# Kernel tuning notes

Measured on AMD Instinct MI355X. Metric: run time of the kernel, lower is better.

The kernel has to match this reference:

```python
import jax, jax.numpy as jnp
import numpy as np

D_MODEL = 1024


def setup_inputs() -> dict:
    key = jax.random.key(0)
    ks = jax.random.split(key, 7)
    B, S, D = 4, 2048, D_MODEL
    scale = 1.0 / np.sqrt(D)
    inp = {
        "query": jax.random.normal(ks[0], (B, S, D), dtype=jnp.float32),
        "key": jax.random.normal(ks[1], (B, S, D), dtype=jnp.float32),
        "value": jax.random.normal(ks[2], (B, S, D), dtype=jnp.float32),
        # NOTE: original torch code applies query_projection to q, k AND v,
        # so only one projection weight (Wq) participates, plus output proj.
        "Wq": (jax.random.normal(ks[3], (D, D), dtype=jnp.float32) * scale),
        "bq": jnp.zeros((D,), dtype=jnp.float32),
        "Wo": (jax.random.normal(ks[4], (D, D), dtype=jnp.float32) * scale),
        "bo": jnp.zeros((D,), dtype=jnp.float32),
    }
    return inp


def reference(query, key, value, Wq, bq, Wo, bo):
    # Faithful to source: same projection (Wq, bq) used for q, k, v.
    q = jnp.einsum("bsd,de->bse", query, Wq) + bq   # (B, S, D)
    k = jnp.einsum("btd,de->bte", key, Wq) + bq     # (B, T, D)
    v = jnp.einsum("btd,de->bte", value, Wq) + bq   # (B, T, D)
    # No 1/sqrt(d) scaling in the original.
    score = jnp.einsum("bse,bte->bst", q, k)        # (B, S, T)
    weights = jax.nn.softmax(score, axis=-1)
    # Dropout is identity in eval / for a deterministic reference.
    ctx = jnp.einsum("bst,bte->bse", weights, v)    # (B, S, D)
    out = jnp.einsum("bse,ef->bsf", ctx, Wo) + bo   # (B, S, D)
    return (out, weights)
```

## Files before the change

kernel.cpp:

```cpp
#include <hip/hip_runtime.h>

typedef unsigned short u16;
typedef unsigned int u32;
typedef signed char i8;
typedef __bf16 bf16x8 __attribute__((ext_vector_type(8)));
typedef float f32x4 __attribute__((ext_vector_type(4)));
typedef int i32x4 __attribute__((ext_vector_type(4)));
typedef i8 i8x4 __attribute__((ext_vector_type(4)));

#define AS1(p) ((const __attribute__((address_space(1))) void*)(p))
#define AS3(p) ((__attribute__((address_space(3))) void*)(p))

__device__ __forceinline__ u16 f2bf(float x) {
  u32 u = __float_as_uint(x);
  u32 r = u + 0x7fffu + ((u >> 16) & 1u);
  return (u16)(r >> 16);
}
__device__ __forceinline__ float bf2f(u16 h) {
  return __uint_as_float(((u32)h) << 16);
}

#define S_IN (8.0f / 127.0f)
#define S_W (0.25f / 127.0f)
#define S_QK (8.0f / 127.0f)
#define INV_S_IN (127.0f / 8.0f)
#define INV_S_W (508.0f)
#define INV_S_QK (127.0f / 8.0f)

__device__ __forceinline__ int2 q8i(float x, float inv_s) {
  float t = fminf(fmaxf(x * inv_s, -126.99f), 126.99f);
  float hf = rintf(t);
  float lf = fminf(fmaxf(rintf((t - hf) * 256.0f), -127.0f), 127.0f);
  return make_int2((int)hf, (int)lf);
}

__global__ __launch_bounds__(256) void split_qk_i8(
    const float* __restrict__ q, const float* __restrict__ k,
    i8* __restrict__ qh, i8* __restrict__ ql, i8* __restrict__ kh,
    i8* __restrict__ kl, int n4) {
  int stride = gridDim.x * blockDim.x;
  for (int i = blockIdx.x * blockDim.x + threadIdx.x; i < n4; i += stride) {
    float4 x = ((const float4*)q)[i];
    float xs[4] = {x.x, x.y, x.z, x.w};
    i8x4 h, l;
#pragma unroll
    for (int e = 0; e < 4; ++e) {
      int2 r = q8i(xs[e], INV_S_IN);
      h[e] = (i8)r.x;
      l[e] = (i8)r.y;
    }
    ((i8x4*)qh)[i] = h;
    ((i8x4*)ql)[i] = l;
    x = ((const float4*)k)[i];
    float ys[4] = {x.x, x.y, x.z, x.w};
#pragma unroll
    for (int e = 0; e < 4; ++e) {
      int2 r = q8i(ys[e], INV_S_IN);
      h[e] = (i8)r.x;
      l[e] = (i8)r.y;
    }
    ((i8x4*)kh)[i] = h;
    ((i8x4*)kl)[i] = l;
  }
}

__global__ void prep_w_i8(const float* __restrict__ Wq,
                          const float* __restrict__ Wo, i8* __restrict__ wqt_h,
                          i8* __restrict__ wqt_l, u16* __restrict__ wot,
                          u16* __restrict__ wq_b, int D) {
  __shared__ float tq[32][33];
  __shared__ float to[32][33];
  int c0 = blockIdx.x * 32, r0 = blockIdx.y * 32;
  int tx = threadIdx.x, ty = threadIdx.y;
#pragma unroll
  for (int i = ty; i < 32; i += 8) {
    float xq = Wq[(size_t)(r0 + i) * D + c0 + tx];
    tq[i][tx] = xq;
    wq_b[(size_t)(r0 + i) * D + c0 + tx] = f2bf(xq);
    to[i][tx] = Wo[(size_t)(r0 + i) * D + c0 + tx];
  }
  __syncthreads();
#pragma unroll
  for (int i = ty; i < 32; i += 8) {
    float x = tq[tx][i];
    int2 r = q8i(x, INV_S_W);
    size_t o = (size_t)(c0 + i) * D + r0 + tx;
    wqt_h[o] = (i8)r.x;
    wqt_l[o] = (i8)r.y;
    wot[o] = f2bf(to[tx][i]);
  }
}

__global__ void transpose_f32_bf16(const float* __restrict__ in,
                                   u16* __restrict__ out, int R, int C) {
  __shared__ float tile[32][33];
  size_t zi = (size_t)blockIdx.z * R * C;
  int c0 = blockIdx.x * 32, r0 = blockIdx.y * 32;
  int tx = threadIdx.x, ty = threadIdx.y;
#pragma unroll
  for (int i = ty; i < 32; i += 8)
    tile[i][tx] = in[zi + (size_t)(r0 + i) * C + (c0 + tx)];
  __syncthreads();
#pragma unroll
  for (int i = ty; i < 32; i += 8)
    out[zi + (size_t)(c0 + i) * R + (r0 + tx)] = f2bf(tile[tx][i]);
}

__global__ __launch_bounds__(256) void bqo_kernel(const float* __restrict__ bq,
                                                  const u16* __restrict__ wot,
                                                  const float* __restrict__ bo,
                                                  float* __restrict__ bqo,
                                                  int D) {
  const int f = blockIdx.x * 4 + (threadIdx.x >> 6);
  const int lane = threadIdx.x & 63;
  const u16* wr_ = wot + (size_t)f * D;
  float s = 0.f;
  for (int e = lane; e < D; e += 64) s += bq[e] * bf2f(wr_[e]);
#pragma unroll
  for (int off = 32; off; off >>= 1) s += __shfl_xor(s, off);
  if (lane == 0) bqo[f] = s + bo[f];
}

template <int EPI>
__global__ __launch_bounds__(256, 2) void gemm_bt(
    const u16* __restrict__ Ah, const u16* __restrict__ Bh,
    const float* __restrict__ bias, float* __restrict__ Cf,
    u16* __restrict__ Ch, int M, int N, int K,
    long long sA, long long sB, long long sC) {
  __shared__ alignas(16) u16 As[128 * 32];
  __shared__ alignas(16) u16 Bs[128 * 32];

  const int t = threadIdx.x;
  const int lane = t & 63;
  const int w = t >> 6;
  const int wr = w >> 1, wc = w & 1;

  const long long zb = blockIdx.z;
  const u16* pA = Ah + zb * sA;
  const u16* pB = Bh + zb * sB;

  const int m0 = blockIdx.x * 128;
  const int n0 = blockIdx.y * 128;

  f32x4 acc[4][4] = {};

  const int row0 = t >> 2;
  const int colS = (t & 3) * 8;
  const int lds0 = (t & ~63) * 8;
  const int lds1 = (256 + (t & ~63)) * 8;

  const size_t aoff0 = (size_t)(m0 + row0) * K + colS;
  const size_t aoff1 = (size_t)(m0 + row0 + 64) * K + colS;
  const size_t boff0 = (size_t)(n0 + row0) * K + colS;
  const size_t boff1 = (size_t)(n0 + row0 + 64) * K + colS;

  for (int k0 = 0; k0 < K; k0 += 32) {
    __syncthreads();
    __builtin_amdgcn_global_load_lds(AS1(pA + aoff0 + k0), AS3(&As[lds0]), 16, 0, 0);
    __builtin_amdgcn_global_load_lds(AS1(pA + aoff1 + k0), AS3(&As[lds1]), 16, 0, 0);
    __builtin_amdgcn_global_load_lds(AS1(pB + boff0 + k0), AS3(&Bs[lds0]), 16, 0, 0);
    __builtin_amdgcn_global_load_lds(AS1(pB + boff1 + k0), AS3(&Bs[lds1]), 16, 0, 0);
    __syncthreads();

    const int fr = lane & 15;
    const int kc = (lane >> 4) * 8;
    bf16x8 a[4], b[4];
#pragma unroll
    for (int i = 0; i < 4; ++i)
      a[i] = *(const bf16x8*)&As[(wr * 64 + i * 16 + fr) * 32 + kc];
#pragma unroll
    for (int j = 0; j < 4; ++j)
      b[j] = *(const bf16x8*)&Bs[(wc * 64 + j * 16 + fr) * 32 + kc];
#pragma unroll
    for (int i = 0; i < 4; ++i)
#pragma unroll
      for (int j = 0; j < 4; ++j)
        acc[i][j] = __builtin_amdgcn_mfma_f32_16x16x32_bf16(a[i], b[j], acc[i][j], 0, 0, 0);
  }

  const int er = (lane >> 4) * 4;
  const int ec = lane & 15;
#pragma unroll
  for (int j = 0; j < 4; ++j) {
    const int gcol = n0 + wc * 64 + j * 16 + ec;
    const float bv = bias ? bias[gcol] : 0.0f;
#pragma unroll
    for (int i = 0; i < 4; ++i) {
      const int grow0 = m0 + wr * 64 + i * 16 + er;
#pragma unroll
      for (int r = 0; r < 4; ++r) {
        const float x = acc[i][j][r] + bv;
        const size_t off = (size_t)zb * sC + (size_t)(grow0 + r) * N + gcol;
        if constexpr (EPI == 0) Cf[off] = x;
        else Ch[off] = f2bf(x);
      }
    }
  }
}

#define PH_PRE()                                                               \
  __builtin_amdgcn_s_barrier();                                                \
  asm volatile("s_waitcnt lgkmcnt(0)" ::: "memory");                           \
  __builtin_amdgcn_s_setprio(1)

#define PH_POST()                                                              \
  __builtin_amdgcn_s_setprio(0);                                               \
  __builtin_amdgcn_s_barrier()

#define STG_I(DSTBASE, SH, SL, ROWBASE, KREAL)                                 \
  do {                                                                         \
    const i8* s0_ = (sc < 4 ? (SH) : (SL)) +                                   \
                    (size_t)((ROWBASE) + sr) * K + (KREAL) + ((sc & 3) << 4);  \
    const i8* s1_ = s0_ + (size_t)64 * K;                                      \
    __builtin_amdgcn_global_load_lds(AS1(s0_), AS3(&lds8[(DSTBASE) + ldsB]), 16, 0, 0); \
    __builtin_amdgcn_global_load_lds(AS1(s1_), AS3(&lds8[(DSTBASE) + 8192 + ldsB]), 16, 0, 0); \
  } while (0)

#define LDA_I(BUF, QM)                                                         \
  do {                                                                         \
    const int base_ = (BUF) * 49152;                                           \
    _Pragma("unroll") for (int i_ = 0; i_ < 4; ++i_) {                         \
      const int r_ = (QM) * 128 + wr * 64 + i_ * 16 + fr;                      \
      ah_[i_] = *(const i32x4*)&lds8[base_ + r_ * 128 + ((ksl ^ (r_ & 7)) << 4)]; \
      al_[i_] = *(const i32x4*)&lds8[base_ + r_ * 128 + (((4 + ksl) ^ (r_ & 7)) << 4)]; \
    }                                                                          \
  } while (0)

#define LDB_I(BUF, J, BH, BL)                                                  \
  do {                                                                         \
    const int base_ = (BUF) * 49152 + 32768;                                   \
    const int r_ = wc * 32 + (J) * 16 + fr;                                    \
    BH = *(const i32x4*)&lds8[base_ + r_ * 128 + ((ksl ^ (r_ & 7)) << 4)];     \
    BL = *(const i32x4*)&lds8[base_ + r_ * 128 + (((4 + ksl) ^ (r_ & 7)) << 4)]; \
  } while (0)

#define MMA_I(QM, J, BH, BL)                                                   \
  do {                                                                         \
    _Pragma("unroll") for (int i_ = 0; i_ < 4; ++i_) {                         \
      accH[(QM) * 4 + i_][J] = __builtin_amdgcn_mfma_i32_16x16x64_i8(          \
          ah_[i_], BH, accH[(QM) * 4 + i_][J], 0, 0, 0);                       \
      accX[(QM) * 4 + i_][J] = __builtin_amdgcn_mfma_i32_16x16x64_i8(          \
          ah_[i_], BL, accX[(QM) * 4 + i_][J], 0, 0, 0);                       \
      accX[(QM) * 4 + i_][J] = __builtin_amdgcn_mfma_i32_16x16x64_i8(          \
          al_[i_], BH, accX[(QM) * 4 + i_][J], 0, 0, 0);                       \
    }                                                                          \
  } while (0)

template <int EPI>
__global__ __launch_bounds__(512, 2) void gemm8i(
    const i8* __restrict__ Ah, const i8* __restrict__ Al,
    const i8* __restrict__ Bh, const i8* __restrict__ Bl,
    const float* __restrict__ bias, float sAB, float* __restrict__ Cf,
    i8* __restrict__ Ch, i8* __restrict__ Cl, int M, int N, int K,
    long long sA, long long sB, long long sC) {
  extern __shared__ i8 lds8[];

  const int tt = threadIdx.x;
  const int lane = tt & 63;
  const int wv = tt >> 6;
  const int wr = wv >> 2;
  const int wc = wv & 3;
  const int fr = lane & 15;
  const int ksl = lane >> 4;

  const long long zb = blockIdx.z;
  const i8* pAh = Ah + zb * sA;
  const i8* pAl = Al + zb * sA;
  const i8* pBh = Bh + zb * sB;
  const i8* pBl = Bl + zb * sB;
  const int m0 = blockIdx.x * 256;
  const int n0 = blockIdx.y * 128;

  const int sr = tt >> 3;
  const int ss = tt & 7;
  const int sc = ss ^ (sr & 7);
  const int ldsB = (tt & ~63) * 16;

  i32x4 accH[8][2] = {};
  i32x4 accX[8][2] = {};
  i32x4 ah_[4], al_[4], b0h, b0l, b1h, b1l;

  const int NT = K / 64;
  const int NITER = NT / 2;

  STG_I(0, pAh, pAl, m0, 0);
  STG_I(16384, pAh, pAl, m0 + 128, 0);
  STG_I(32768, pBh, pBl, n0, 0);
  STG_I(49152, pAh, pAl, m0, 64);
  asm volatile("s_waitcnt vmcnt(2)" ::: "memory");
  __builtin_amdgcn_s_barrier();
  __builtin_amdgcn_sched_barrier(0);

  for (int it = 0; it < NITER; ++it) {
    const int t0 = 2 * it;
    const int k1 = (t0 + 1) * 64;
    const int k2 = (t0 + 2 < NT ? t0 + 2 : NT - 1) * 64;
    const int k3 = (t0 + 3 < NT ? t0 + 3 : NT - 1) * 64;

    LDA_I(0, 0);
    LDB_I(0, 0, b0h, b0l);
    STG_I(49152 + 16384, pAh, pAl, m0 + 128, k1);
    PH_PRE();
    MMA_I(0, 0, b0h, b0l);
    PH_POST();

    LDB_I(0, 1, b1h, b1l);
    STG_I(49152 + 32768, pBh, pBl, n0, k1);
    PH_PRE();
    MMA_I(0, 1, b1h, b1l);
    PH_POST();

    LDA_I(0, 1);
    STG_I(0, pAh, pAl, m0, k2);
    PH_PRE();
    MMA_I(1, 0, b0h, b0l);
    PH_POST();

    PH_PRE();
    MMA_I(1, 1, b1h, b1l);
    __builtin_amdgcn_s_setprio(0);
    asm volatile("s_waitcnt vmcnt(2)" ::: "memory");
    __builtin_amdgcn_s_barrier();
    __builtin_amdgcn_sched_barrier(0);

    LDA_I(1, 0);
    LDB_I(1, 0, b0h, b0l);
    STG_I(16384, pAh, pAl, m0 + 128, k2);
    PH_PRE();
    MMA_I(0, 0, b0h, b0l);
    PH_POST();

    LDB_I(1, 1, b1h, b1l);
    STG_I(32768, pBh, pBl, n0, k2);
    PH_PRE();
    MMA_I(0, 1, b1h, b1l);
    PH_POST();

    LDA_I(1, 1);
    STG_I(49152, pAh, pAl, m0, k3);
    PH_PRE();
    MMA_I(1, 0, b0h, b0l);
    PH_POST();

    PH_PRE();
    MMA_I(1, 1, b1h, b1l);
    __builtin_amdgcn_s_setprio(0);
    asm volatile("s_waitcnt vmcnt(2)" ::: "memory");
    __builtin_amdgcn_s_barrier();
    __builtin_amdgcn_sched_barrier(0);
  }

  const int er = (lane >> 4) * 4;
  const int ec = lane & 15;
#pragma unroll
  for (int fi = 0; fi < 8; ++fi) {
    const int grow0 = m0 + (fi >> 2) * 128 + wr * 64 + (fi & 3) * 16 + er;
#pragma unroll
    for (int j = 0; j < 2; ++j) {
      const int gcol = n0 + wc * 32 + j * 16 + ec;
      const float bv = bias ? bias[gcol] : 0.0f;
#pragma unroll
      for (int r = 0; r < 4; ++r) {
        const float x =
            sAB * ((float)accH[fi][j][r] + (float)accX[fi][j][r] * 0.00390625f) + bv;
        const size_t off = (size_t)zb * sC + (size_t)(grow0 + r) * N + gcol;
        if constexpr (EPI == 0) {
          Cf[off] = x;
        } else {
          int2 qq = q8i(x, INV_S_QK);
          Ch[off] = (i8)qq.x;
          Cl[off] = (i8)qq.y;
        }
      }
    }
  }
}

#define STG_P(DSTBASE, SRC, ROWBASE, KREAL)                                    \
  do {                                                                         \
    const u16* s0_ = (SRC) + (size_t)((ROWBASE) + sr) * K + (KREAL) + (sc << 3); \
    const u16* s1_ = s0_ + (size_t)64 * K;                                     \
    __builtin_amdgcn_global_load_lds(AS1(s0_), AS3(&lds[(DSTBASE) + ldsW]), 16, 0, 0); \
    __builtin_amdgcn_global_load_lds(AS1(s1_), AS3(&lds[(DSTBASE) + 4096 + ldsW]), 16, 0, 0); \
  } while (0)

#define LDA_P(BUF, QM, S)                                                      \
  do {                                                                         \
    const int base_ = (BUF) * 24576 + (QM) * 8192;                             \
    _Pragma("unroll") for (int i_ = 0; i_ < 4; ++i_) {                         \
      const int r_ = wr * 64 + i_ * 16 + fr;                                   \
      a[i_] = *(const bf16x8*)&lds[base_ + r_ * 64 + (((((S) * 4 + ksl)) ^ (r_ & 7)) << 3)]; \
    }                                                                          \
  } while (0)

#define LDB_P(BUF, S)                                                          \
  do {                                                                         \
    const int base_ = (BUF) * 24576 + 16384;                                   \
    _Pragma("unroll") for (int j_ = 0; j_ < 2; ++j_) {                         \
      const int r_ = wc * 32 + j_ * 16 + fr;                                   \
      b[j_] = *(const bf16x8*)&lds[base_ + r_ * 64 + (((((S) * 4 + ksl)) ^ (r_ & 7)) << 3)]; \
    }                                                                          \
  } while (0)

#define MMA_P(QM)                                                              \
  do {                                                                         \
    _Pragma("unroll") for (int i_ = 0; i_ < 4; ++i_) {                         \
      _Pragma("unroll") for (int j_ = 0; j_ < 2; ++j_) {                       \
        acc[(QM) * 4 + i_][j_] = __builtin_amdgcn_mfma_f32_16x16x32_bf16(      \
            a[i_], b[j_], acc[(QM) * 4 + i_][j_], 0, 0, 0);                    \
      }                                                                        \
    }                                                                          \
  } while (0)

template <int EPI>
__global__ __launch_bounds__(512, 2) void gemm8p(
    const u16* __restrict__ A, const u16* __restrict__ B,
    const float* __restrict__ bias, float* __restrict__ Cf,
    u16* __restrict__ Ch, int M, int N, int K,
    long long sA, long long sB, long long sC) {
  extern __shared__ u16 lds[];

  const int tt = threadIdx.x;
  const int lane = tt & 63;
  const int wv = tt >> 6;
  const int wr = wv >> 2;
  const int wc = wv & 3;
  const int fr = lane & 15;
  const int ksl = lane >> 4;

  const long long zb = blockIdx.z;
  const u16* pA = A + zb * sA;
  const u16* pB = B + zb * sB;
  const int m0 = blockIdx.x * 256;
  const int n0 = blockIdx.y * 128;

  const int sr = tt >> 3;
  const int ss = tt & 7;
  const int sc = ss ^ (sr & 7);
  const int ldsW = (tt & ~63) * 8;

  f32x4 acc[8][2] = {};
  bf16x8 a[4], b[2];

  const int NT = K / 64;

  STG_P(16384, pB, n0, 0);
  STG_P(0, pA, m0, 0);
  STG_P(8192, pA, m0 + 128, 0);
  asm volatile("s_waitcnt vmcnt(2)" ::: "memory");
  __builtin_amdgcn_s_barrier();
  __builtin_amdgcn_sched_barrier(0);

  for (int it = 0; it < NT; ++it) {
    const int cur = it & 1;
    const int nb = (cur ^ 1) * 24576;
    const int kn = (it + 1 < NT ? it + 1 : NT - 1) * 64;

    LDA_P(cur, 0, 0);
    LDB_P(cur, 0);
    STG_P(nb + 16384, pB, n0, kn);
    PH_PRE();
    MMA_P(0);
    __builtin_amdgcn_s_setprio(0);
    asm volatile("s_waitcnt vmcnt(2)" ::: "memory");
    __builtin_amdgcn_s_barrier();
    __builtin_amdgcn_sched_barrier(0);

    LDA_P(cur, 1, 0);
    STG_P(nb + 0, pA, m0, kn);
    PH_PRE();
    MMA_P(1);
    PH_POST();

    LDA_P(cur, 0, 1);
    LDB_P(cur, 1);
    STG_P(nb + 8192, pA, m0 + 128, kn);
    PH_PRE();
    MMA_P(0);
    PH_POST();

    LDA_P(cur, 1, 1);
    PH_PRE();
    MMA_P(1);
    __builtin_amdgcn_s_setprio(0);
    asm volatile("s_waitcnt vmcnt(2)" ::: "memory");
    __builtin_amdgcn_s_barrier();
    __builtin_amdgcn_sched_barrier(0);
  }

  const int er = (lane >> 4) * 4;
  const int ec = lane & 15;
#pragma unroll
  for (int fi = 0; fi < 8; ++fi) {
    const int qm = fi >> 2, i = fi & 3;
    const int grow0 = m0 + qm * 128 + wr * 64 + i * 16 + er;
#pragma unroll
    for (int j = 0; j < 2; ++j) {
      const int gcol = n0 + wc * 32 + j * 16 + ec;
      const float bv = bias ? bias[gcol] : 0.0f;
#pragma unroll
      for (int r = 0; r < 4; ++r) {
        const float x = acc[fi][j][r] + bv;
        const size_t off = (size_t)zb * sC + (size_t)(grow0 + r) * N + gcol;
        if constexpr (EPI == 0) Cf[off] = x;
        else Ch[off] = f2bf(x);
      }
    }
  }
}

__global__ __launch_bounds__(256) void softmax_rows(float* __restrict__ S,
                                                    u16* __restrict__ P) {
  const int T = 2048;
  const size_t row = blockIdx.x;
  float* sr = S + row * T;
  u16* pr = P + row * T;
  const int t = threadIdx.x;
  const int w = t >> 6, lane = t & 63;
  __shared__ float red[8];

  float v[8];
  float mx = -1e30f;
#pragma unroll
  for (int i = 0; i < 8; ++i) {
    v[i] = sr[t + 256 * i];
    mx = fmaxf(mx, v[i]);
  }
#pragma unroll
  for (int off = 32; off; off >>= 1) mx = fmaxf(mx, __shfl_xor(mx, off));
  if (lane == 0) red[w] = mx;
  __syncthreads();
  mx = fmaxf(fmaxf(red[0], red[1]), fmaxf(red[2], red[3]));

  float s = 0.f;
#pragma unroll
  for (int i = 0; i < 8; ++i) {
    v[i] = __expf(v[i] - mx);
    s += v[i];
  }
#pragma unroll
  for (int off = 32; off; off >>= 1) s += __shfl_xor(s, off);
  if (lane == 0) red[4 + w] = s;
  __syncthreads();
  s = (red[4] + red[5]) + (red[6] + red[7]);
  const float inv = 1.0f / s;
#pragma unroll
  for (int i = 0; i < 8; ++i) {
    const float wv = v[i] * inv;
    sr[t + 256 * i] = wv;
    pr[t + 256 * i] = f2bf(wv);
  }
}

extern "C" void kernel_launch(void* const* d_in, const int* in_sizes, int n_in,
                              void* d_out, int out_size, void* d_ws,
                              size_t ws_size, hipStream_t stream) {
  (void)in_sizes; (void)n_in; (void)out_size; (void)ws_size;
  const float* query = (const float*)d_in[0];
  const float* key   = (const float*)d_in[1];
  const float* value = (const float*)d_in[2];
  const float* Wq    = (const float*)d_in[3];
  const float* bq    = (const float*)d_in[4];
  const float* Wo    = (const float*)d_in[5];
  const float* bo    = (const float*)d_in[6];

  const int S = 2048, D = 1024;
  const size_t n = (size_t)4 * S * D;

  float* out = (float*)d_out;
  float* wts = out + n;

  char* ws = (char*)d_ws;
  i8* wqt_h = (i8*)(ws);
  i8* wqt_l = (i8*)(ws + (1ull << 20));
  u16* wot  = (u16*)(ws + (2ull << 20));
  u16* wq_b = (u16*)(ws + (4ull << 20));
  u16* wqoT = (u16*)(ws + (6ull << 20));
  float* bqo = (float*)(ws + (8ull << 20));
  i8* QKh = (i8*)(ws + (9ull << 20));
  i8* QKl = (i8*)(ws + (25ull << 20));
  u16* tmp = (u16*)(ws + (41ull << 20));
  u16* P = (u16*)(ws + (9ull << 20));

  i8* ah = (i8*)wts;
  i8* al = ah + 2 * n;
  u16* valT = (u16*)out;

  hipFuncSetAttribute((const void*)&gemm8i<2>,
                      hipFuncAttributeMaxDynamicSharedMemorySize, 98304);
  hipFuncSetAttribute((const void*)&gemm8i<0>,
                      hipFuncAttributeMaxDynamicSharedMemorySize, 98304);
  hipFuncSetAttribute((const void*)&gemm8p<1>,
                      hipFuncAttributeMaxDynamicSharedMemorySize, 98304);
  hipFuncSetAttribute((const void*)&gemm8p<0>,
                      hipFuncAttributeMaxDynamicSharedMemorySize, 98304);

  split_qk_i8<<<2048, 256, 0, stream>>>(query, key, ah, al, ah + n, al + n,
                                        (int)(n / 4));
  prep_w_i8<<<dim3(D / 32, D / 32), dim3(32, 8), 0, stream>>>(
      Wq, Wo, wqt_h, wqt_l, wot, wq_b, D);
  transpose_f32_bf16<<<dim3(D / 32, S / 32, 4), dim3(32, 8), 0, stream>>>(
      value, valT, S, D);
  gemm_bt<1><<<dim3(8, 8, 1), 256, 0, stream>>>(
      wot, wq_b, nullptr, nullptr, wqoT, 1024, 1024, 1024, 0, 0, 0);
  bqo_kernel<<<256, 256, 0, stream>>>(bq, wot, bo, bqo, D);
  gemm8i<2><<<dim3(64, 8, 1), 512, 98304, stream>>>(
      ah, al, wqt_h, wqt_l, bq, S_IN * S_W, nullptr, QKh, QKl,
      16384, 1024, 1024, 0, 0, 0);
  gemm8i<0><<<dim3(8, 16, 4), 512, 98304, stream>>>(
      QKh, QKl, QKh + n, QKl + n, nullptr, S_QK * S_QK, wts, nullptr, nullptr,
      2048, 2048, 1024, (long long)S * D, (long long)S * D, (long long)S * S);
  softmax_rows<<<8192, 256, 0, stream>>>(wts, P);
  gemm8p<1><<<dim3(8, 8, 4), 512, 98304, stream>>>(
      P, valT, nullptr, nullptr, tmp, 2048, 1024, 2048, (long long)S * S,
      (long long)D * S, (long long)S * D);
  gemm8p<0><<<dim3(32, 8, 1), 512, 98304, stream>>>(
      tmp, wqoT, bqo, out, nullptr, 8192, 1024, 1024, 0, 0, 0);
}
```

Before: 273.7 us.

## Coarsen GEMM k-loop phases to batch LDS fragment loads before larger MFMA blocks

```diff
diff --git a/kernel.cpp b/kernel.cpp
--- a/kernel.cpp
+++ b/kernel.cpp
@@ -226,23 +226,27 @@
     }                                                                          \
   } while (0)
 
-#define LDB_I(BUF, J, BH, BL)                                                  \
+#define LDB_I2(BUF)                                                            \
   do {                                                                         \
     const int base_ = (BUF) * 49152 + 32768;                                   \
-    const int r_ = wc * 32 + (J) * 16 + fr;                                    \
-    BH = *(const i32x4*)&lds8[base_ + r_ * 128 + ((ksl ^ (r_ & 7)) << 4)];     \
-    BL = *(const i32x4*)&lds8[base_ + r_ * 128 + (((4 + ksl) ^ (r_ & 7)) << 4)]; \
-  } while (0)
-
-#define MMA_I(QM, J, BH, BL)                                                   \
-  do {                                                                         \
-    _Pragma("unroll") for (int i_ = 0; i_ < 4; ++i_) {                         \
-      accH[(QM) * 4 + i_][J] = __builtin_amdgcn_mfma_i32_16x16x64_i8(          \
-          ah_[i_], BH, accH[(QM) * 4 + i_][J], 0, 0, 0);                       \
-      accX[(QM) * 4 + i_][J] = __builtin_amdgcn_mfma_i32_16x16x64_i8(          \
-          ah_[i_], BL, accX[(QM) * 4 + i_][J], 0, 0, 0);                       \
-      accX[(QM) * 4 + i_][J] = __builtin_amdgcn_mfma_i32_16x16x64_i8(          \
-          al_[i_], BH, accX[(QM) * 4 + i_][J], 0, 0, 0);                       \
+    _Pragma("unroll") for (int j_ = 0; j_ < 2; ++j_) {                         \
+      const int r_ = wc * 32 + j_ * 16 + fr;                                   \
+      bh[j_] = *(const i32x4*)&lds8[base_ + r_ * 128 + ((ksl ^ (r_ & 7)) << 4)]; \
+      bl[j_] = *(const i32x4*)&lds8[base_ + r_ * 128 + (((4 + ksl) ^ (r_ & 7)) << 4)]; \
+    }                                                                          \
+  } while (0)
+
+#define MMA_I2(QM)                                                             \
+  do {                                                                         \
+    _Pragma("unroll") for (int j_ = 0; j_ < 2; ++j_) {                         \
+      _Pragma("unroll") for (int i_ = 0; i_ < 4; ++i_) {                       \
+        accH[(QM) * 4 + i_][j_] = __builtin_amdgcn_mfma_i32_16x16x64_i8(       \
+            ah_[i_], bh[j_], accH[(QM) * 4 + i_][j_], 0, 0, 0);                \
+        accX[(QM) * 4 + i_][j_] = __builtin_amdgcn_mfma_i32_16x16x64_i8(       \
+            ah_[i_], bl[j_], accX[(QM) * 4 + i_][j_], 0, 0, 0);                \
+        accX[(QM) * 4 + i_][j_] = __builtin_amdgcn_mfma_i32_16x16x64_i8(       \
+            al_[i_], bh[j_], accX[(QM) * 4 + i_][j_], 0, 0, 0);                \
+      }                                                                        \
     }                                                                          \
   } while (0)
 
@@ -278,7 +282,7 @@
 
   i32x4 accH[8][2] = {};
   i32x4 accX[8][2] = {};
-  i32x4 ah_[4], al_[4], b0h, b0l, b1h, b1l;
+  i32x4 ah_[4], al_[4], bh[2], bl[2];
 
   const int NT = K / 64;
   const int NITER = NT / 2;
@@ -298,52 +302,34 @@
     const int k3 = (t0 + 3 < NT ? t0 + 3 : NT - 1) * 64;
 
     LDA_I(0, 0);
-    LDB_I(0, 0, b0h, b0l);
+    LDB_I2(0);
     STG_I(49152 + 16384, pAh, pAl, m0 + 128, k1);
-    PH_PRE();
-    MMA_I(0, 0, b0h, b0l);
-    PH_POST();
-
-    LDB_I(0, 1, b1h, b1l);
     STG_I(49152 + 32768, pBh, pBl, n0, k1);
     PH_PRE();
-    MMA_I(0, 1, b1h, b1l);
+    MMA_I2(0);
     PH_POST();
 
     LDA_I(0, 1);
     STG_I(0, pAh, pAl, m0, k2);
     PH_PRE();
-    MMA_I(1, 0, b0h, b0l);
-    PH_POST();
-
-    PH_PRE();
-    MMA_I(1, 1, b1h, b1l);
+    MMA_I2(1);
     __builtin_amdgcn_s_setprio(0);
     asm volatile("s_waitcnt vmcnt(2)" ::: "memory");
     __builtin_amdgcn_s_barrier();
     __builtin_amdgcn_sched_barrier(0);
 
     LDA_I(1, 0);
-    LDB_I(1, 0, b0h, b0l);
+    LDB_I2(1);
     STG_I(16384, pAh, pAl, m0 + 128, k2);
-    PH_PRE();
-    MMA_I(0, 0, b0h, b0l);
-    PH_POST();
-
-    LDB_I(1, 1, b1h, b1l);
     STG_I(32768, pBh, pBl, n0, k2);
     PH_PRE();
-    MMA_I(0, 1, b1h, b1l);
+    MMA_I2(0);
     PH_POST();
 
     LDA_I(1, 1);
     STG_I(49152, pAh, pAl, m0, k3);
     PH_PRE();
-    MMA_I(1, 0, b0h, b0l);
-    PH_POST();
-
-    PH_PRE();
-    MMA_I(1, 1, b1h, b1l);
+    MMA_I2(1);
     __builtin_amdgcn_s_setprio(0);
     asm volatile("s_waitcnt vmcnt(2)" ::: "memory");
     __builtin_amdgcn_s_barrier();
@@ -384,30 +370,30 @@
     __builtin_amdgcn_global_load_lds(AS1(s1_), AS3(&lds[(DSTBASE) + 4096 + ldsW]), 16, 0, 0); \
   } while (0)
 
-#define LDA_P(BUF, QM, S)                                                      \
+#define LDA_P(BUF, QM, S, DST)                                                 \
   do {                                                                         \
     const int base_ = (BUF) * 24576 + (QM) * 8192;                             \
     _Pragma("unroll") for (int i_ = 0; i_ < 4; ++i_) {                         \
       const int r_ = wr * 64 + i_ * 16 + fr;                                   \
-      a[i_] = *(const bf16x8*)&lds[base_ + r_ * 64 + (((((S) * 4 + ksl)) ^ (r_ & 7)) << 3)]; \
+      DST[i_] = *(const bf16x8*)&lds[base_ + r_ * 64 + (((((S) * 4 + ksl)) ^ (r_ & 7)) << 3)]; \
     }                                                                          \
   } while (0)
 
-#define LDB_P(BUF, S)                                                          \
+#define LDB_P(BUF, S, DST)                                                     \
   do {                                                                         \
     const int base_ = (BUF) * 24576 + 16384;                                   \
     _Pragma("unroll") for (int j_ = 0; j_ < 2; ++j_) {                         \
       const int r_ = wc * 32 + j_ * 16 + fr;                                   \
-      b[j_] = *(const bf16x8*)&lds[base_ + r_ * 64 + (((((S) * 4 + ksl)) ^ (r_ & 7)) << 3)]; \
+      DST[j_] = *(const bf16x8*)&lds[base_ + r_ * 64 + (((((S) * 4 + ksl)) ^ (r_ & 7)) << 3)]; \
     }                                                                          \
   } while (0)
 
-#define MMA_P(QM)                                                              \
+#define MMA_P(QM, A_, B_)                                                      \
   do {                                                                         \
     _Pragma("unroll") for (int i_ = 0; i_ < 4; ++i_) {                         \
       _Pragma("unroll") for (int j_ = 0; j_ < 2; ++j_) {                       \
         acc[(QM) * 4 + i_][j_] = __builtin_amdgcn_mfma_f32_16x16x32_bf16(      \
-            a[i_], b[j_], acc[(QM) * 4 + i_][j_], 0, 0, 0);                    \
+            A_[i_], B_[j_], acc[(QM) * 4 + i_][j_], 0, 0, 0);                  \
       }                                                                        \
     }                                                                          \
   } while (0)
@@ -440,7 +426,7 @@
   const int ldsW = (tt & ~63) * 8;
 
   f32x4 acc[8][2] = {};
-  bf16x8 a[4], b[2];
+  bf16x8 a0[4], a1[4], b0[2], b1[2];
 
   const int NT = K / 64;
 
@@ -456,32 +442,26 @@
     const int nb = (cur ^ 1) * 24576;
     const int kn = (it + 1 < NT ? it + 1 : NT - 1) * 64;
 
-    LDA_P(cur, 0, 0);
-    LDB_P(cur, 0);
+    LDA_P(cur, 0, 0, a0);
+    LDA_P(cur, 0, 1, a1);
+    LDB_P(cur, 0, b0);
+    LDB_P(cur, 1, b1);
     STG_P(nb + 16384, pB, n0, kn);
+    STG_P(nb + 0, pA, m0, kn);
     PH_PRE();
-    MMA_P(0);
+    MMA_P(0, a0, b0);
+    MMA_P(0, a1, b1);
     __builtin_amdgcn_s_setprio(0);
-    asm volatile("s_waitcnt vmcnt(2)" ::: "memory");
+    asm volatile("s_waitcnt vmcnt(4)" ::: "memory");
     __builtin_amdgcn_s_barrier();
     __builtin_amdgcn_sched_barrier(0);
 
-    LDA_P(cur, 1, 0);
-    STG_P(nb + 0, pA, m0, kn);
-    PH_PRE();
-    MMA_P(1);
-    PH_POST();
-
-    LDA_P(cur, 0, 1);
-    LDB_P(cur, 1);
+    LDA_P(cur, 1, 0, a0);
+    LDA_P(cur, 1, 1, a1);
     STG_P(nb + 8192, pA, m0 + 128, kn);
     PH_PRE();
-    MMA_P(0);
-    PH_POST();
-
-    LDA_P(cur, 1, 1);
-    PH_PRE();
-    MMA_P(1);
+    MMA_P(1, a0, b0);
+    MMA_P(1, a1, b1);
     __builtin_amdgcn_s_setprio(0);
     asm volatile("s_waitcnt vmcnt(2)" ::: "memory");
     __builtin_amdgcn_s_barrier();
```

After: 275.2 us. No clear change (+0.5%).
